# Optimization experiments

Hardware: AMD Instinct MI355X
Metric: run time of the kernel (lower is better)

The kernel has to match this reference:

```python
import jax, jax.numpy as jnp
import numpy as np
from jax import lax

NMS_TH = 0.05
TOPK_P = 1000
NMS_IOU = 0.5
NUMDETS = 100
NMS_ITERS = 15
IM = 2048.0
SIZES = [256, 128, 64, 32, 16]
NUM_CLASS = 80


def _make_boxes(key, n):
    k1, k2, k3, k4 = jax.random.split(key, 4)
    cy = jax.random.uniform(k1, (n,)) * IM
    cx = jax.random.uniform(k2, (n,)) * IM
    h = jax.random.uniform(k3, (n,)) * 300.0 + 16.0
    w = jax.random.uniform(k4, (n,)) * 300.0 + 16.0
    # yxyx boxes
    return jnp.stack([cy - h / 2, cx - w / 2, cy + h / 2, cx + w / 2], axis=1)


def setup_inputs() -> dict:
    key = jax.random.key(0)
    inp = {}
    for s, sz in enumerate(SIZES):
        kc = jax.random.fold_in(key, 2 * s)
        kb = jax.random.fold_in(key, 2 * s + 1)
        n = sz * sz
        inp['cls%d' % s] = jax.random.normal(kc, (1, n, NUM_CLASS), jnp.float32) - 2.0
        inp['reg%d' % s] = _make_boxes(kb, n)[None]
    inp['locations'] = jnp.array([0.0, 0.0, IM - 1.0, IM - 1.0, 1024.0, 1024.0], jnp.float32)
    return inp


def _pairwise_iou(a, b):
    # a: (N,4) yxyx, b: (M,4) yxyx -> (N,M)
    area_a = jnp.clip(a[:, 2] - a[:, 0], 0) * jnp.clip(a[:, 3] - a[:, 1], 0)
    area_b = jnp.clip(b[:, 2] - b[:, 0], 0) * jnp.clip(b[:, 3] - b[:, 1], 0)
    iy1 = jnp.maximum(a[:, None, 0], b[None, :, 0])
    ix1 = jnp.maximum(a[:, None, 1], b[None, :, 1])
    iy2 = jnp.minimum(a[:, None, 2], b[None, :, 2])
    ix2 = jnp.minimum(a[:, None, 3], b[None, :, 3])
    inter = jnp.clip(iy2 - iy1, 0) * jnp.clip(ix2 - ix1, 0)
    union = area_a[:, None] + area_b[None, :] - inter
    return inter / jnp.maximum(union, 1e-9)


def _cluster_nms(boxes, scores, classes, valid, iou_th):
    order = jnp.argsort(-scores)
    b = boxes[order]
    s = scores[order]
    c = classes[order]
    v = valid[order]
    iou = jnp.triu(_pairwise_iou(b, b), k=1)  # (K,K)

    def body(B, _):
        max_a = B.max(axis=0)
        keep_col = (max_a <= iou_th).astype(B.dtype)[:, None]
        return iou * keep_col, None

    B, _ = lax.scan(body, iou, None, length=NMS_ITERS)
    keep = (B.max(axis=0) <= iou_th) & v
    return b, s, c, keep


def _per_level(cls_s, reg_s):
    p = jax.nn.sigmoid(cls_s[0])                 # (N, C)
    ps = p.max(axis=1)                           # (N,)
    pi = p.argmax(axis=1).astype(jnp.int32) + 1  # class index, 0 is background
    m = ps > NMS_TH
    ps_m = jnp.where(m, ps, -1.0)
    k = min(TOPK_P, ps_m.shape[0])
    top_s, top_idx = lax.top_k(ps_m, k)
    return top_s, pi[top_idx], reg_s[0][top_idx], m[top_idx]


def reference(cls0, cls1, cls2, cls3, cls4, reg0, reg1, reg2, reg3, reg4, locations):
    levels = [(cls0, reg0), (cls1, reg1), (cls2, reg2), (cls3, reg3), (cls4, reg4)]
    sc, cl, bx, vd = [], [], [], []
    for cls_s, reg_s in levels:
        s_, c_, b_, v_ = _per_level(cls_s, reg_s)
        sc.append(s_); cl.append(c_); bx.append(b_); vd.append(v_)
    scores = jnp.concatenate(sc)
    classes = jnp.concatenate(cl)
    boxes = jnp.concatenate(bx, axis=0)
    valid = jnp.concatenate(vd)
    scores = jnp.where(valid, scores, 0.0)

    vy1, vx1, vy2, vx2 = locations[0], locations[1], locations[2], locations[3]
    ori_h, ori_w = locations[4], locations[5]
    boxes = jnp.stack([
        jnp.maximum(boxes[:, 0], vy1), jnp.maximum(boxes[:, 1], vx1),
        jnp.minimum(boxes[:, 2], vy2), jnp.minimum(boxes[:, 3], vx2)], axis=1)

    b, s, c, keep = _cluster_nms(boxes, scores, classes, valid, NMS_IOU)
    s = jnp.where(keep, s, 0.0)
    top_s, sel = lax.top_k(s, NUMDETS)
    bbox = b[sel]
    cls_out = c[sel]

    # transfer boxes back to original-image coordinates
    sy = ori_h / jnp.maximum(vy2 - vy1, 1e-6)
    sx = ori_w / jnp.maximum(vx2 - vx1, 1e-6)
    bbox = jnp.stack([
        (bbox[:, 0] - vy1) * sy, (bbox[:, 1] - vx1) * sx,
        (bbox[:, 2] - vy1) * sy, (bbox[:, 3] - vx1) * sx], axis=1)
    return bbox, cls_out, top_s
```

## Files before the change

### kernel.cpp

```cpp
#include <hip/hip_runtime.h>
#include <math.h>

#define NANCH 87296
#define NF 4256
#define CAPD 128
#define NBINS 65536
#define NITER 16
#define BCAP 2048
#define EC 8192
#define NBLK 341
#define BIN_NEG 0x407Fu

struct InPtrs {
    const float* cls[5];
    const float* reg[5];
    const float* loc;
};

constexpr size_t SZ_HIST  = 5ull * NBINS * 4;
constexpr size_t OFF_HIST = 0;
constexpr size_t OFF_CNT  = OFF_HIST + SZ_HIST;
constexpr size_t OFF_CTR  = OFF_CNT + (size_t)NF * 4;
constexpr size_t ZERO_SZ  = OFF_CTR + 64;
constexpr size_t OFF_SBITS = ((ZERO_SZ + 255) / 256) * 256;
constexpr size_t OFF_CLSV  = OFF_SBITS + (size_t)NANCH * 4;
constexpr size_t OFF_PAR   = OFF_CLSV + (size_t)NANCH * 4;
constexpr size_t OFF_INVB  = OFF_PAR + 128;
constexpr size_t OFF_INVO  = OFF_INVB + (size_t)NBLK * 4;
constexpr size_t OFF_FINK  = ((OFF_INVO + (size_t)NBLK * 4 + 255) / 256) * 256;
constexpr size_t OFF_BBUF  = OFF_FINK + (size_t)NF * 8;
constexpr size_t OFF_SBOX  = OFF_BBUF + 5ull * BCAP * 8;
constexpr size_t OFF_SSC   = OFF_SBOX + (size_t)NF * 16;
constexpr size_t OFF_SCV   = OFF_SSC + (size_t)NF * 4;
constexpr size_t OFF_SAR   = OFF_SCV + (size_t)NF * 4;
constexpr size_t OFF_NBR   = OFF_SAR + (size_t)NF * 4;

__device__ __forceinline__ void lvl_of(int a, int& lev, int& idx) {
    if (a < 65536)      { lev = 0; idx = a; }
    else if (a < 81920) { lev = 1; idx = a - 65536; }
    else if (a < 86016) { lev = 2; idx = a - 81920; }
    else if (a < 87040) { lev = 3; idx = a - 86016; }
    else                { lev = 4; idx = a - 87040; }
}

__device__ __forceinline__ unsigned int fkey(float f) {
    unsigned int u = __float_as_uint(f);
    return u ^ ((u & 0x80000000u) ? 0xFFFFFFFFu : 0x80000000u);
}
__device__ __forceinline__ float funkey(unsigned int k) {
    return __uint_as_float(k ^ ((k & 0x80000000u) ? 0x80000000u : 0xFFFFFFFFu));
}
__device__ __forceinline__ unsigned int binaddr(unsigned int bin) {
    return ((bin & 63u) << 10) | (bin >> 6);
}

__global__ __launch_bounds__(1024) void k1_score(InPtrs P, unsigned int* hist,
        unsigned int* sbits, unsigned int* clsv, unsigned int* invBlk) {
    int t = threadIdx.x;
    int a = blockIdx.x * 256 + (t >> 2);
    int k = t & 3;
    int lev, idx; lvl_of(a, lev, idx);
    const float4* row = (const float4*)(P.cls[lev] + (size_t)idx * 80);
    float best = -INFINITY; int bi = 0;
    #pragma unroll
    for (int q = 0; q < 5; ++q) {
        float4 v = row[q * 4 + k];
        int c0 = q * 16 + k * 4;
        if (v.x > best) { best = v.x; bi = c0 + 0; }
        if (v.y > best) { best = v.y; bi = c0 + 1; }
        if (v.z > best) { best = v.z; bi = c0 + 2; }
        if (v.w > best) { best = v.w; bi = c0 + 3; }
    }
    #pragma unroll
    for (int m = 1; m < 4; m <<= 1) {
        float ob = __shfl_xor(best, m, 64);
        int  obi = __shfl_xor(bi, m, 64);
        if (ob > best || (ob == best && obi < bi)) { best = ob; bi = obi; }
    }
    bool lead = (k == 0);
    unsigned int valid = 0;
    if (lead) {
        float score = 1.0f / (1.0f + expf(-best));
        valid = (score > 0.05f) ? 1u : 0u;
        float psm = valid ? score : -1.0f;
        unsigned int sb = fkey(psm);
        sbits[a] = sb;
        clsv[a] = (unsigned int)(bi + 1) | (valid << 31);
        if (valid) atomicAdd(&hist[(size_t)lev * NBINS + binaddr(sb >> 16)], 1u);
    }
    __shared__ unsigned int wv[16];
    unsigned long long mv = __ballot(lead && valid);
    int lane = t & 63, w = t >> 6;
    if (lane == 0) wv[w] = (unsigned int)__popcll(mv);
    __syncthreads();
    if (t == 0) {
        unsigned int s = 0;
        #pragma unroll
        for (int i = 0; i < 16; ++i) s += wv[i];
        invBlk[blockIdx.x] = 256u - s;
    }
}

__global__ __launch_bounds__(1024) void k2_scan(const unsigned int* hist,
        const unsigned int* invBlk, unsigned int* params, unsigned int* invOff) {
    int t = threadIdx.x;
    if (blockIdx.x == 5) {
        __shared__ unsigned int sv[512];
        __shared__ unsigned int orig[512];
        if (t < 512) {
            unsigned int v = (t < NBLK) ? invBlk[t] : 0u;
            sv[t] = v; orig[t] = v;
        }
        __syncthreads();
        for (int off = 1; off < 512; off <<= 1) {
            unsigned int add = 0;
            if (t < 512 && t >= off) add = sv[t - off];
            __syncthreads();
            if (t < 512) sv[t] += add;
            __syncthreads();
        }
        if (t < NBLK) {
            int segStart = (t < 256) ? 0 : (t < 320) ? 256 : (t < 336) ? 320
                         : (t < 340) ? 336 : 340;
            invOff[t] = sv[t] - orig[t] - (segStart > 0 ? sv[segStart - 1] : 0u);
        }
        return;
    }
    int lev = blockIdx.x;
    unsigned int K = (lev == 4) ? 256u : 1000u;
    const unsigned int* h = hist + (size_t)lev * NBINS;
    __shared__ unsigned int seg[1024];
    __shared__ unsigned int suf[1024];
    unsigned int s = 0;
    #pragma unroll 8
    for (int q = 0; q < 64; ++q) s += h[(q << 10) | t];
    seg[t] = s;
    suf[t] = s;
    __syncthreads();
    for (int off = 1; off < 1024; off <<= 1) {
        unsigned int v = suf[t];
        unsigned int add = (t + off < 1024) ? suf[t + off] : 0u;
        __syncthreads();
        suf[t] = v + add;
        __syncthreads();
    }
    unsigned int totValid = suf[0];
    if (totValid >= K) {
        unsigned int excl = suf[t] - seg[t];
        if (excl < K && excl + seg[t] >= K) {
            unsigned int cum = excl;
            for (int b = 63; b >= 0; --b) {
                unsigned int c = h[(b << 10) | t];
                if (cum + c >= K) {
                    params[lev] = (unsigned int)(t * 64 + b);
                    params[8 + lev] = K - cum;
                    params[16 + lev] = 0;
                    break;
                }
                cum += c;
            }
        }
    } else if (t == 0) {
        params[lev] = BIN_NEG;
        params[8 + lev] = 0;
        params[16 + lev] = K - totValid;
    }
}

__global__ __launch_bounds__(256) void k3_compact(const unsigned int* sbits,
        const unsigned int* clsv, const unsigned int* params,
        const unsigned int* invOff, unsigned long long* finKeys,
        unsigned int* ctrs, unsigned long long* bBuf) {
    int blk = blockIdx.x;
    int t = threadIdx.x;
    int a = blk * 256 + t;
    int lev, idx; lvl_of(a, lev, idx);
    unsigned int sb = sbits[a];
    unsigned int cv = clsv[a];
    unsigned int h16 = sb >> 16;
    unsigned int Bs = params[lev];
    unsigned int rNeg = params[16 + lev];
    unsigned int valid = cv >> 31;
    int lane = t & 63, w = t >> 6;
    unsigned long long lt = (1ull << lane) - 1ull;
    __shared__ unsigned int wInv[4], wFin[4], wB[4];
    __shared__ unsigned int baseFin, baseB;
    unsigned long long mInv = __ballot(valid == 0u);
    if (lane == 0) wInv[w] = (unsigned int)__popcll(mInv);
    __syncthreads();
    unsigned int invRank = invOff[blk] + (unsigned int)__popcll(mInv & lt);
    for (int i = 0; i < w; ++i) invRank += wInv[i];
    bool isFin, isB;
    if (valid) {
        isFin = (h16 > Bs);
        isB   = (h16 == Bs);
    } else {
        isFin = (Bs == BIN_NEG) && (invRank < rNeg);
        isB   = false;
    }
    unsigned long long mFin = __ballot(isFin);
    unsigned long long mB   = __ballot(isB);
    if (lane == 0) { wFin[w] = (unsigned int)__popcll(mFin); wB[w] = (unsigned int)__popcll(mB); }
    __syncthreads();
    if (t == 0) {
        unsigned int tf = wFin[0] + wFin[1] + wFin[2] + wFin[3];
        unsigned int tb = wB[0] + wB[1] + wB[2] + wB[3];
        baseFin = tf ? atomicAdd(&ctrs[0], tf) : 0u;
        baseB   = tb ? atomicAdd(&ctrs[1 + lev], tb) : 0u;
    }
    __syncthreads();
    if (isFin || isB) {
        unsigned int composite = ((unsigned int)lev << 16) | (unsigned int)idx;
        unsigned int inv = (~composite) & 0x7FFFFu;
        unsigned int low = (inv << 13) | (valid << 7) | (cv & 0x7Fu);
        unsigned long long key = ((unsigned long long)sb << 32) | low;
        if (isFin) {
            unsigned int p = baseFin + (unsigned int)__popcll(mFin & lt);
            for (int i = 0; i < w; ++i) p += wFin[i];
            if (p < NF) finKeys[p] = key;
        } else {
            unsigned int p = baseB + (unsigned int)__popcll(mB & lt);
            for (int i = 0; i < w; ++i) p += wB[i];
            if (p < BCAP) bBuf[(size_t)lev * BCAP + p] = key;
        }
    }
}

__global__ __launch_bounds__(256) void k5_rank(InPtrs P,
        const unsigned long long* finKeys, const unsigned int* ctrs,
        const unsigned int* params, const unsigned long long* bBuf,
        float4* sBox, float* sScore, unsigned int* sCV, float* sArea) {
    __shared__ __align__(16) unsigned long long keys[NF];
    __shared__ __align__(16) unsigned long long kb[BCAP];
    __shared__ unsigned int rnk[64];
    __shared__ unsigned int posS;
    int t = threadIdx.x;
    unsigned int fc = ctrs[0];
    if (fc > NF) fc = NF;
    for (int i = t; i < (int)fc; i += 256) keys[i] = finKeys[i];
    if (t < 64) rnk[t] = 0;
    if (t == 0) posS = fc;
    __syncthreads();
    for (int lev = 0; lev < 5; ++lev) {
        unsigned int bc = ctrs[1 + lev];
        int n = (bc > BCAP) ? BCAP : (int)bc;
        int r = (int)params[8 + lev];
        if (r > n) r = n;
        if (r > 0) {
            for (int i = t; i < n; i += 256) kb[i] = bBuf[(size_t)lev * BCAP + i];
            __syncthreads();
            for (int i = t; i < n; i += 256) {
                unsigned long long my = kb[i];
                unsigned int c = 0;
                #pragma unroll 4
                for (int j = 0; j < n; ++j) c += (kb[j] > my) ? 1u : 0u;
                if (c < (unsigned int)r) {
                    unsigned int p = atomicAdd(&posS, 1u);
                    if (p < NF) keys[p] = my;
                }
            }
            __syncthreads();
        }
    }
    unsigned int pos = posS;
    for (int i = (int)pos + t; i < NF; i += 256) keys[i] = (unsigned long long)i;
    __syncthreads();
    int lf = t & 63;
    int seg = t >> 6;
    int f = blockIdx.x * 64 + lf;
    unsigned long long my = (f < NF) ? keys[f] : ~0ull;
    {
        unsigned int c = 0;
        const ulonglong2* kp = (const ulonglong2*)keys + seg * 532;
        #pragma unroll 4
        for (int i = 0; i < 532; ++i) {
            ulonglong2 v = kp[i];
            c += (v.x > my) ? 1u : 0u;
            c += (v.y > my) ? 1u : 0u;
        }
        atomicAdd(&rnk[lf], c);
    }
    __syncthreads();
    if (seg == 0 && f < NF) {
        unsigned int r = rnk[lf];
        unsigned int sb  = (unsigned int)(my >> 32);
        unsigned int low = (unsigned int)my;
        unsigned int composite = (~(low >> 13)) & 0x7FFFFu;
        int lev = composite >> 16;
        int idx = composite & 0xFFFF;
        float4 b = ((const float4*)P.reg[lev])[idx];
        float vy1 = P.loc[0], vx1 = P.loc[1], vy2 = P.loc[2], vx2 = P.loc[3];
        float y1 = fmaxf(b.x, vy1), x1 = fmaxf(b.y, vx1);
        float y2 = fminf(b.z, vy2), x2 = fminf(b.w, vx2);
        float area = __fmul_rn(fmaxf(y2 - y1, 0.0f), fmaxf(x2 - x1, 0.0f));
        unsigned int valid = (low >> 7) & 1u;
        sBox[r] = make_float4(y1, x1, y2, x2);
        sScore[r] = valid ? funkey(sb) : 0.0f;
        sCV[r] = (low & 0x7Fu) | (valid << 31);
        sArea[r] = area;
    }
}

__global__ __launch_bounds__(256) void k6_adj(const float4* sBox,
        const float* sArea, unsigned int* cnt, unsigned short* nbr) {
    int L = blockIdx.x;
    float fr = sqrtf(8.0f * (float)L + 1.0f);
    int jt = (int)((fr - 1.0f) * 0.5f);
    while ((jt + 1) * (jt + 2) / 2 <= L) jt++;
    while (jt * (jt + 1) / 2 > L) jt--;
    int it = L - jt * (jt + 1) / 2;
    __shared__ float4 cb[64]; __shared__ float ca[64];
    __shared__ float4 rb[64]; __shared__ float ra[64];
    int t = threadIdx.x;
    if (t < 64) {
        int j = jt * 64 + t;
        if (j < NF) { cb[t] = sBox[j]; ca[t] = sArea[j]; }
        int i = it * 64 + t;
        if (i < NF) { rb[t] = sBox[i]; ra[t] = sArea[i]; }
    }
    __syncthreads();
    int lj = t & 63;
    int j = jt * 64 + lj;
    if (j >= NF) return;
    float4 B = cb[lj]; float ab = ca[lj];
    for (int li = (t >> 6); li < 64; li += 4) {
        int i = it * 64 + li;
        if (i >= j) continue;
        float4 A = rb[li]; float aa = ra[li];
        float iy1 = fmaxf(A.x, B.x), ix1 = fmaxf(A.y, B.y);
        float iy2 = fminf(A.z, B.z), ix2 = fminf(A.w, B.w);
        float ih = fmaxf(iy2 - iy1, 0.0f), iw = fmaxf(ix2 - ix1, 0.0f);
        float inter = __fmul_rn(ih, iw);
        float uni = __fsub_rn(__fadd_rn(aa, ab), inter);
        float iou = __fdiv_rn(inter, fmaxf(uni, 1e-9f));
        if (iou > 0.5f) {
            unsigned int p = atomicAdd(&cnt[j], 1u);
            if (p < CAPD) nbr[(size_t)j * CAPD + p] = (unsigned short)i;
        }
    }
}

__global__ __launch_bounds__(1024) void k7_nms(InPtrs P, const float4* sBox,
        const float* sScore, const unsigned int* sCV, const unsigned int* cnt,
        const unsigned short* nbr, float* out) {
    __shared__ unsigned int off[NF + 1];
    __shared__ unsigned int edges[EC];
    __shared__ __align__(4) unsigned char bufA[NF];
    __shared__ __align__(4) unsigned char bufB[NF];
    __shared__ unsigned int csum[1024];
    __shared__ float ploc[6];
    int t = threadIdx.x;
    if (t < 6) ploc[t] = P.loc[t];
    const int CH = 5;
    unsigned int dq[CH];
    {
        unsigned int s = 0;
        #pragma unroll
        for (int q = 0; q < CH; ++q) {
            int j = t * CH + q;
            unsigned int d = 0;
            if (j < NF) { d = cnt[j]; if (d > CAPD) d = CAPD; }
            dq[q] = d; s += d;
        }
        csum[t] = s;
        for (int j = t; j < NF; j += 1024) bufA[j] = 1;
        __syncthreads();
        for (int o = 1; o < 1024; o <<= 1) {
            unsigned int v = csum[t];
            unsigned int add = (t >= o) ? csum[t - o] : 0u;
            __syncthreads();
            csum[t] = v + add;
            __syncthreads();
        }
        unsigned int base = csum[t] - s;
        #pragma unroll
        for (int q = 0; q < CH; ++q) {
            int j = t * CH + q;
            if (j < NF) { off[j] = base; base += dq[q]; }
        }
        if (t == 1023) off[NF] = csum[1023];
    }
    __syncthreads();
    unsigned int E = off[NF];
    bool useLds = (E <= (unsigned int)EC);
    if (useLds) {
        #pragma unroll
        for (int q = 0; q < CH; ++q) {
            int j = t * CH + q;
            if (j < NF) {
                unsigned int o = off[j];
                unsigned int d = dq[q];
                const unsigned short* nl = nbr + (size_t)j * CAPD;
                for (unsigned int e = 0; e < d; ++e)
                    edges[o + e] = ((unsigned int)nl[e] << 16) | (unsigned int)j;
            }
        }
    }
    __syncthreads();
    unsigned char* cur = bufA; unsigned char* nxt = bufB;
    if (useLds) {
        for (int itr = 0; itr < NITER; ++itr) {
            if (t < (NF + 3) / 4) ((unsigned int*)nxt)[t] = 0x01010101u;
            __syncthreads();
            for (int e = t; e < (int)E; e += 1024) {
                unsigned int pk = edges[e];
                if (cur[pk >> 16]) nxt[pk & 0xFFFFu] = 0;
            }
            __syncthreads();
            unsigned char* tm = cur; cur = nxt; nxt = tm;
        }
    } else {
        for (int itr = 0; itr < NITER; ++itr) {
            for (int j = t; j < NF; j += 1024) {
                unsigned int d = cnt[j]; if (d > CAPD) d = CAPD;
                const unsigned short* nl = nbr + (size_t)j * CAPD;
                unsigned char kp = 1;
                for (unsigned int e = 0; e < d; ++e)
                    if (cur[nl[e]]) { kp = 0; break; }
                nxt[j] = kp;
            }
            __syncthreads();
            unsigned char* tm = cur; cur = nxt; nxt = tm;
        }
    }
    int base = t * CH;
    unsigned char kf[CH];
    unsigned int sum = 0;
    #pragma unroll
    for (int q = 0; q < CH; ++q) {
        int j = base + q;
        unsigned char v = 0;
        if (j < NF) v = cur[j] & (unsigned char)(sCV[j] >> 31);
        kf[q] = v; sum += v;
    }
    csum[t] = sum;
    __syncthreads();
    for (int o = 1; o < 1024; o <<= 1) {
        unsigned int v = csum[t];
        unsigned int add = (t >= o) ? csum[t - o] : 0u;
        __syncthreads();
        csum[t] = v + add;
        __syncthreads();
    }
    unsigned int keptTot = csum[1023];
    unsigned int run = csum[t] - sum;
    float vy1 = ploc[0], vx1 = ploc[1], vy2 = ploc[2], vx2 = ploc[3];
    float sy = ploc[4] / fmaxf(vy2 - vy1, 1e-6f);
    float sx = ploc[5] / fmaxf(vx2 - vx1, 1e-6f);
    #pragma unroll
    for (int q = 0; q < CH; ++q) {
        int j = base + q;
        if (j >= NF) break;
        unsigned int slot = 0xFFFFFFFFu;
        float sc = 0.0f;
        if (kf[q]) {
            if (run < 100u) { slot = run; sc = sScore[j]; }
            run++;
        } else if (keptTot < 100u) {
            unsigned int nk = (unsigned int)j - run;
            unsigned int s2 = keptTot + nk;
            if (s2 < 100u) { slot = s2; sc = 0.0f; }
        }
        if (slot < 100u) {
            float4 b = sBox[j];
            out[slot * 4 + 0] = (b.x - vy1) * sy;
            out[slot * 4 + 1] = (b.y - vx1) * sx;
            out[slot * 4 + 2] = (b.z - vy1) * sy;
            out[slot * 4 + 3] = (b.w - vx1) * sx;
            out[400 + slot] = (float)(sCV[j] & 0x7Fu);
            out[500 + slot] = sc;
        }
    }
}

extern "C" void kernel_launch(void* const* d_in, const int* in_sizes, int n_in,
                              void* d_out, int out_size, void* d_ws, size_t ws_size,
                              hipStream_t stream) {
    (void)n_in; (void)out_size; (void)ws_size;
    InPtrs P;
    bool inter = (in_sizes[1] == 65536 * 4);
    for (int s = 0; s < 5; ++s) {
        P.cls[s] = (const float*)d_in[inter ? 2 * s : s];
        P.reg[s] = (const float*)d_in[inter ? 2 * s + 1 : 5 + s];
    }
    P.loc = (const float*)d_in[10];

    char* w = (char*)d_ws;
    unsigned int* hist   = (unsigned int*)(w + OFF_HIST);
    unsigned int* cnt    = (unsigned int*)(w + OFF_CNT);
    unsigned int* ctrs   = (unsigned int*)(w + OFF_CTR);
    unsigned int* sbits  = (unsigned int*)(w + OFF_SBITS);
    unsigned int* clsv   = (unsigned int*)(w + OFF_CLSV);
    unsigned int* params = (unsigned int*)(w + OFF_PAR);
    unsigned int* invBlk = (unsigned int*)(w + OFF_INVB);
    unsigned int* invOff = (unsigned int*)(w + OFF_INVO);
    unsigned long long* finKeys = (unsigned long long*)(w + OFF_FINK);
    unsigned long long* bBuf    = (unsigned long long*)(w + OFF_BBUF);
    float4* sBox  = (float4*)(w + OFF_SBOX);
    float* sScore = (float*)(w + OFF_SSC);
    unsigned int* sCV = (unsigned int*)(w + OFF_SCV);
    float* sArea  = (float*)(w + OFF_SAR);
    unsigned short* nbr = (unsigned short*)(w + OFF_NBR);

    hipMemsetAsync(d_ws, 0, ZERO_SZ, stream);
    k1_score<<<NBLK, 1024, 0, stream>>>(P, hist, sbits, clsv, invBlk);
    k2_scan<<<6, 1024, 0, stream>>>(hist, invBlk, params, invOff);
    k3_compact<<<NBLK, 256, 0, stream>>>(sbits, clsv, params, invOff, finKeys, ctrs, bBuf);
    k5_rank<<<67, 256, 0, stream>>>(P, finKeys, ctrs, params, bBuf, sBox, sScore, sCV, sArea);
    k6_adj<<<2278, 256, 0, stream>>>(sBox, sArea, cnt, nbr);
    k7_nms<<<1, 1024, 0, stream>>>(P, sBox, sScore, sCV, cnt, nbr, (float*)d_out);
}
```

Before: 187.7 us.

## Use finer 24-bit score histogram restricted to valid sigmoid range for top-k threshold

```diff
diff --git a/kernel.cpp b/kernel.cpp
--- a/kernel.cpp
+++ b/kernel.cpp
@@ -4,12 +4,13 @@
 #define NANCH 87296
 #define NF 4256
 #define CAPD 128
-#define NBINS 65536
 #define NITER 16
-#define BCAP 2048
+#define BCAP 512
 #define EC 8192
 #define NBLK 341
-#define BIN_NEG 0x407Fu
+#define BIN_BASE 0xBD4C00u
+#define NB24 147456
+#define BPT 144
 
 struct InPtrs {
     const float* cls[5];
@@ -17,7 +18,7 @@
     const float* loc;
 };
 
-constexpr size_t SZ_HIST  = 5ull * NBINS * 4;
+constexpr size_t SZ_HIST  = 5ull * NB24 * 4;
 constexpr size_t OFF_HIST = 0;
 constexpr size_t OFF_CNT  = OFF_HIST + SZ_HIST;
 constexpr size_t OFF_CTR  = OFF_CNT + (size_t)NF * 4;
@@ -50,8 +51,10 @@
 __device__ __forceinline__ float funkey(unsigned int k) {
     return __uint_as_float(k ^ ((k & 0x80000000u) ? 0x80000000u : 0xFFFFFFFFu));
 }
-__device__ __forceinline__ unsigned int binaddr(unsigned int bin) {
-    return ((bin & 63u) << 10) | (bin >> 6);
+__device__ __forceinline__ unsigned int bin24_addr(unsigned int v) {
+    unsigned int owner = v / BPT;
+    unsigned int i = v - owner * BPT;
+    return (i << 10) | owner;
 }
 
 __global__ __launch_bounds__(1024) void k1_score(InPtrs P, unsigned int* hist,
@@ -86,7 +89,10 @@
         unsigned int sb = fkey(psm);
         sbits[a] = sb;
         clsv[a] = (unsigned int)(bi + 1) | (valid << 31);
-        if (valid) atomicAdd(&hist[(size_t)lev * NBINS + binaddr(sb >> 16)], 1u);
+        if (valid) {
+            unsigned int bin = (sb >> 8) - BIN_BASE;
+            atomicAdd(&hist[(size_t)lev * NB24 + bin24_addr(bin)], 1u);
+        }
     }
     __shared__ unsigned int wv[16];
     unsigned long long mv = __ballot(lead && valid);
@@ -128,12 +134,12 @@
     }
     int lev = blockIdx.x;
     unsigned int K = (lev == 4) ? 256u : 1000u;
-    const unsigned int* h = hist + (size_t)lev * NBINS;
+    const unsigned int* h = hist + (size_t)lev * NB24;
     __shared__ unsigned int seg[1024];
     __shared__ unsigned int suf[1024];
     unsigned int s = 0;
     #pragma unroll 8
-    for (int q = 0; q < 64; ++q) s += h[(q << 10) | t];
+    for (int i = 0; i < BPT; ++i) s += h[(i << 10) | t];
     seg[t] = s;
     suf[t] = s;
     __syncthreads();
@@ -149,10 +155,10 @@
         unsigned int excl = suf[t] - seg[t];
         if (excl < K && excl + seg[t] >= K) {
             unsigned int cum = excl;
-            for (int b = 63; b >= 0; --b) {
-                unsigned int c = h[(b << 10) | t];
+            for (int i = BPT - 1; i >= 0; --i) {
+                unsigned int c = h[(i << 10) | t];
                 if (cum + c >= K) {
-                    params[lev] = (unsigned int)(t * 64 + b);
+                    params[lev] = (unsigned int)(t * BPT + i);
                     params[8 + lev] = K - cum;
                     params[16 + lev] = 0;
                     break;
@@ -161,7 +167,7 @@
             }
         }
     } else if (t == 0) {
-        params[lev] = BIN_NEG;
+        params[lev] = 0;
         params[8 + lev] = 0;
         params[16 + lev] = K - totValid;
     }
@@ -177,7 +183,7 @@
     int lev, idx; lvl_of(a, lev, idx);
     unsigned int sb = sbits[a];
     unsigned int cv = clsv[a];
-    unsigned int h16 = sb >> 16;
+    unsigned int bin = (sb >> 8) - BIN_BASE;
     unsigned int Bs = params[lev];
     unsigned int rNeg = params[16 + lev];
     unsigned int valid = cv >> 31;
@@ -192,10 +198,10 @@
     for (int i = 0; i < w; ++i) invRank += wInv[i];
     bool isFin, isB;
     if (valid) {
-        isFin = (h16 > Bs);
-        isB   = (h16 == Bs);
+        isFin = (bin > Bs);
+        isB   = (bin == Bs);
     } else {
-        isFin = (Bs == BIN_NEG) && (invRank < rNeg);
+        isFin = (rNeg > 0) && (invRank < rNeg);
         isB   = false;
     }
     unsigned long long mFin = __ballot(isFin);
@@ -252,7 +258,6 @@
             for (int i = t; i < n; i += 256) {
                 unsigned long long my = kb[i];
                 unsigned int c = 0;
-                #pragma unroll 4
                 for (int j = 0; j < n; ++j) c += (kb[j] > my) ? 1u : 0u;
                 if (c < (unsigned int)r) {
                     unsigned int p = atomicAdd(&posS, 1u);
```

Result: no change. 185.6 us (-1.1%).
